# Kernel tuning notes

Measured on AMD Instinct MI355X. Metric: run time of the kernel, lower is better.

The kernel has to match this reference:

```python
import jax, jax.numpy as jnp
import numpy as np
import math

B, T, C = 2, 2048, 1024
H = 16
D = C // H


def setup_inputs() -> dict:
    key = jax.random.key(0)
    ks = jax.random.split(key, 5)
    s = 1.0 / math.sqrt(C)
    return {
        "x": jax.random.normal(ks[0], (B, T, C), dtype=jnp.float32),
        "W_qkv": jax.random.normal(ks[1], (C, 3 * C), dtype=jnp.float32) * s,
        "b_qkv": jnp.zeros((3 * C,), dtype=jnp.float32),
        "W_proj": jax.random.normal(ks[2], (C, C), dtype=jnp.float32) * s,
        "b_proj": jnp.zeros((C,), dtype=jnp.float32),
    }


def reference(x, W_qkv, b_qkv, W_proj, b_proj):
    qkv = x @ W_qkv + b_qkv  # [B,T,3C]
    q, k, v = jnp.split(qkv, 3, axis=-1)
    # [B,T,C] -> [B,H,T,D]
    q = q.reshape(B, T, H, D).transpose(0, 2, 1, 3)
    k = k.reshape(B, T, H, D).transpose(0, 2, 1, 3)
    v = v.reshape(B, T, H, D).transpose(0, 2, 1, 3)
    sm_scale = 1.0 / math.sqrt(D)
    att = jnp.einsum("bhqd,bhkd->bhqk", q, k) * sm_scale
    causal = jnp.tril(jnp.ones((T, T), dtype=bool))  # True = keep
    att = jnp.where(causal, att, -jnp.inf)
    att = jax.nn.softmax(att, axis=-1)
    y = jnp.einsum("bhqk,bhkd->bhqd", att, v)  # [B,H,T,D]
    y = y.transpose(0, 2, 1, 3).reshape(B, T, C)
    return y @ W_proj + b_proj
```

## Files before the change

kernel.cpp:

```cpp
#include <hip/hip_runtime.h>
#include <hip/hip_bf16.h>
#include <math.h>

#define BB 2
#define TT 2048
#define CCH 1024
#define HH 16
#define DD 64
#define BT (BB*TT)
#define N3 (3*CCH)

typedef __attribute__((ext_vector_type(8))) short short8;
typedef __attribute__((ext_vector_type(4))) float f32x4;
typedef __attribute__((ext_vector_type(16))) float f32x16;

__device__ __forceinline__ unsigned short f2bf(float f) {
  unsigned int u = __float_as_uint(f);
  unsigned int r = (u + 0x7FFFu + ((u >> 16) & 1u)) >> 16;
  return (unsigned short)r;
}
__device__ __forceinline__ int cvtpk(float lo, float hi) {
  int r;
  asm("v_cvt_pk_bf16_f32 %0, %1, %2" : "=v"(r) : "v"(lo), "v"(hi));
  return r;
}
__device__ __forceinline__ void plswap(int &a, int &b) {
  asm("v_permlane32_swap_b32 %0, %1" : "+v"(a), "+v"(b));
}
__device__ __forceinline__ float fexp2(float x) {
  float r;
  asm("v_exp_f32 %0, %1" : "=v"(r) : "v"(x));
  return r;
}
__device__ __forceinline__ void gload_lds16(const unsigned short* g, unsigned short* l) {
  __builtin_amdgcn_global_load_lds((const __attribute__((address_space(1))) void*)g,
                                   (__attribute__((address_space(3))) void*)l, 16, 0, 0);
}
__device__ __forceinline__ float fmax3(float a, float b, float c) {
  return fmaxf(fmaxf(a, b), c);
}

__global__ __launch_bounds__(256) void k_convert(const float* __restrict__ in,
                                                 unsigned short* __restrict__ out, int n8) {
  int i = blockIdx.x * 256 + threadIdx.x;
  if (i < n8) {
    const float4 a = *(const float4*)(in + (size_t)i * 8);
    const float4 b = *(const float4*)(in + (size_t)i * 8 + 4);
    short8 v;
    v[0] = f2bf(a.x); v[1] = f2bf(a.y); v[2] = f2bf(a.z); v[3] = f2bf(a.w);
    v[4] = f2bf(b.x); v[5] = f2bf(b.y); v[6] = f2bf(b.z); v[7] = f2bf(b.w);
    *(short8*)(out + (size_t)i * 8) = v;
  }
}

__global__ __launch_bounds__(256) void k_transpose_cvt(const float* __restrict__ in,
                                                       unsigned short* __restrict__ out,
                                                       int R, int Cn) {
  __shared__ float tile[32][33];
  int tc = blockIdx.x * 32;
  int tr = blockIdx.y * 32;
  int lx = threadIdx.x & 31;
  int ly = threadIdx.x >> 5;
#pragma unroll
  for (int i = 0; i < 32; i += 8)
    tile[ly + i][lx] = in[(size_t)(tr + ly + i) * Cn + tc + lx];
  __syncthreads();
#pragma unroll
  for (int i = 0; i < 32; i += 8)
    out[(size_t)(tc + ly + i) * R + tr + lx] = f2bf(tile[lx][ly + i]);
}

__global__ __launch_bounds__(256) void k_qkv_gemm(const unsigned short* __restrict__ Xb,
                                                  const unsigned short* __restrict__ Wt,
                                                  const float* __restrict__ bias,
                                                  unsigned short* __restrict__ Qo,
                                                  unsigned short* __restrict__ Ko,
                                                  unsigned short* __restrict__ Vto) {
  __shared__ __align__(16) unsigned short As[128 * 32];
  __shared__ __align__(16) unsigned short Bs[128 * 32];
  int tid = threadIdx.x;
  int mb = blockIdx.x * 128;
  int nb = blockIdx.y * 128;
  int wid = tid >> 6, lane = tid & 63;
  int wr = (wid >> 1) * 64, wc = (wid & 1) * 64;
  int l15 = lane & 15, l4 = lane >> 4;
  int l16 = lane >> 2, lc = (lane & 3) * 8;
  f32x4 acc[4][4];
#pragma unroll
  for (int a = 0; a < 4; ++a)
#pragma unroll
    for (int b = 0; b < 4; ++b)
#pragma unroll
      for (int j = 0; j < 4; ++j) acc[a][b][j] = 0.0f;

  for (int kb = 0; kb < CCH; kb += 32) {
#pragma unroll
    for (int i = 0; i < 2; ++i) {
      int arow = wid * 32 + i * 16;
      gload_lds16(Xb + (size_t)(mb + arow + l16) * CCH + kb + lc, &As[arow * 32]);
      gload_lds16(Wt + (size_t)(nb + arow + l16) * CCH + kb + lc, &Bs[arow * 32]);
    }
    __syncthreads();
    short8 af[4], bfr[4];
#pragma unroll
    for (int mt = 0; mt < 4; ++mt) af[mt] = *(const short8*)(&As[(wr + mt * 16 + l15) * 32 + l4 * 8]);
#pragma unroll
    for (int nt = 0; nt < 4; ++nt) bfr[nt] = *(const short8*)(&Bs[(wc + nt * 16 + l15) * 32 + l4 * 8]);
#pragma unroll
    for (int mt = 0; mt < 4; ++mt)
#pragma unroll
      for (int nt = 0; nt < 4; ++nt)
        acc[mt][nt] = __builtin_amdgcn_mfma_f32_16x16x32_bf16(af[mt], bfr[nt], acc[mt][nt], 0, 0, 0);
    __syncthreads();
  }

#pragma unroll
  for (int mt = 0; mt < 4; ++mt) {
#pragma unroll
    for (int nt = 0; nt < 4; ++nt) {
      int gcol = nb + wc + nt * 16 + l15;
      int which = gcol >> 10;
      int cc = gcol & 1023;
      int h = cc >> 6, d = cc & 63;
      float bv = bias[gcol];
#pragma unroll
      for (int j = 0; j < 4; ++j) {
        int grow = mb + wr + mt * 16 + l4 * 4 + j;
        int b = grow >> 11, t = grow & 2047;
        float v = acc[mt][nt][j] + bv;
        size_t bh = (size_t)(b * HH + h);
        if (which == 0)      Qo[(bh * TT + t) * DD + d] = f2bf(v * 0.18033688f);
        else if (which == 1) Ko[(bh * TT + t) * DD + d] = f2bf(v);
        else                 Vto[(bh * DD + d) * TT + t] = f2bf(v);
      }
    }
  }
}

__global__ __launch_bounds__(128) void k_attn(const unsigned short* __restrict__ Qb,
                                              const unsigned short* __restrict__ Kb,
                                              const unsigned short* __restrict__ Vtb,
                                              unsigned short* __restrict__ Y) {
  __shared__ __align__(16) unsigned short Ks[2][64 * 64];
  __shared__ __align__(16) unsigned short Vs[2][64 * 64];
  int tid = threadIdx.x;
  int jx = blockIdx.x;
  int qsub = 31 - (jx >> 5);
  int bh = jx & 31;

  const unsigned short* Qp = Qb + (size_t)bh * TT * DD;
  const unsigned short* Kp = Kb + (size_t)bh * TT * DD;
  const unsigned short* Vp = Vtb + (size_t)bh * DD * TT;
  int wid = tid >> 6, lane = tid & 63;
  int l31 = lane & 31, h = lane >> 5;
  int q0 = qsub * 64 + wid * 32;
  int qrow = q0 + l31;

  short8 qf[4];
#pragma unroll
  for (int m = 0; m < 4; ++m)
    qf[m] = *(const short8*)(Qp + (size_t)qrow * DD + m * 16 + h * 8);

  f32x16 zv;
#pragma unroll
  for (int r = 0; r < 16; ++r) zv[r] = 0.0f;
  f32x16 po[2];
  po[0] = zv; po[1] = zv;
  float mrun = -1e30f, lrun = 0.0f;

#pragma unroll
  for (int i2 = 0; i2 < 4; ++i2) {
    int c = i2 * 128 + wid * 64 + lane;
    int srow = c >> 3, scol = ((c & 7) ^ (srow & 7)) * 8;
    int dst = (i2 * 128 + wid * 64) * 8;
    gload_lds16(Kp + (size_t)srow * DD + scol, &Ks[0][dst]);
    gload_lds16(Vp + (size_t)srow * TT + scol, &Vs[0][dst]);
  }

  int buf = 0;
  for (int t = 0; t <= qsub; ++t) {
    __syncthreads();
    int kvb = t * 64;
    if (t < qsub) {
      int kvb2 = kvb + 64;
#pragma unroll
      for (int i2 = 0; i2 < 4; ++i2) {
        int c = i2 * 128 + wid * 64 + lane;
        int srow = c >> 3, scol = ((c & 7) ^ (srow & 7)) * 8;
        int dst = (i2 * 128 + wid * 64) * 8;
        gload_lds16(Kp + (size_t)(kvb2 + srow) * DD + scol, &Ks[buf ^ 1][dst]);
        gload_lds16(Vp + (size_t)srow * TT + kvb2 + scol, &Vs[buf ^ 1][dst]);
      }
    }

    {
      f32x16 st[2];
      __builtin_amdgcn_s_setprio(1);
#pragma unroll
      for (int t32 = 0; t32 < 2; ++t32) {
        int row = t32 * 32 + l31;
        {
          int off = row * 64 + ((h ^ (row & 7)) * 8);
          short8 kf = *(const short8*)(&Ks[buf][off]);
          st[t32] = __builtin_amdgcn_mfma_f32_32x32x16_bf16(kf, qf[0], zv, 0, 0, 0);
        }
#pragma unroll
        for (int m = 1; m < 4; ++m) {
          int off = row * 64 + (((2 * m + h) ^ (row & 7)) * 8);
          short8 kf = *(const short8*)(&Ks[buf][off]);
          st[t32] = __builtin_amdgcn_mfma_f32_32x32x16_bf16(kf, qf[m], st[t32], 0, 0, 0);
        }
      }
      __builtin_amdgcn_s_setprio(0);

      if (kvb + 63 > q0) {
#pragma unroll
        for (int t32 = 0; t32 < 2; ++t32)
#pragma unroll
          for (int r = 0; r < 16; ++r) {
            int kvg = kvb + t32 * 32 + (r & 3) + 8 * (r >> 2) + 4 * h;
            if (kvg > qrow) st[t32][r] = -1e30f;
          }
      }

      float A = st[0][0], B = st[0][1], C = st[0][2], Dv = st[0][3];
#pragma unroll
      for (int r = 4; r < 16; r += 4) {
        A = fmax3(A, st[0][r], st[0][r + 1]);
        B = fmax3(B, st[0][r + 2], st[0][r + 3]);
        C = fmax3(C, st[1][r - 4], st[1][r - 3]);
        Dv = fmax3(Dv, st[1][r - 2], st[1][r - 1]);
      }
      C = fmax3(C, st[1][12], st[1][13]);
      Dv = fmax3(Dv, st[1][14], st[1][15]);
      float mx = fmaxf(fmax3(A, B, C), Dv);
      mx = fmaxf(mx, __shfl_xor(mx, 32));

      if (__any(mx - mrun > 8.0f)) {
        float mnew = fmaxf(mrun, mx);
        float alpha = fexp2(mrun - mnew);
        lrun *= alpha;
#pragma unroll
        for (int dt = 0; dt < 2; ++dt)
#pragma unroll
          for (int r = 0; r < 16; ++r) po[dt][r] *= alpha;
        mrun = mnew;
      }

      float sum = 0.0f;
#pragma unroll
      for (int t32 = 0; t32 < 2; ++t32)
#pragma unroll
        for (int r = 0; r < 16; ++r) {
          float p = fexp2(st[t32][r] - mrun);
          st[t32][r] = p;
          sum += p;
        }
      sum += __shfl_xor(sum, 32);
      lrun += sum;

      short8 pf[4];
#pragma unroll
      for (int g = 0; g < 4; ++g) {
        int t32 = g >> 1, r0 = (g & 1) * 8;
        int a = cvtpk(st[t32][r0 + 0], st[t32][r0 + 1]);
        int b = cvtpk(st[t32][r0 + 4], st[t32][r0 + 5]);
        plswap(a, b);
        int c = cvtpk(st[t32][r0 + 2], st[t32][r0 + 3]);
        int d = cvtpk(st[t32][r0 + 6], st[t32][r0 + 7]);
        plswap(c, d);
        union { int w[4]; short8 s; } un;
        un.w[0] = a; un.w[1] = c; un.w[2] = b; un.w[3] = d;
        pf[g] = un.s;
      }

      __builtin_amdgcn_s_setprio(1);
#pragma unroll
      for (int dt = 0; dt < 2; ++dt) {
#pragma unroll
        for (int g = 0; g < 4; ++g) {
          int row = dt * 32 + l31;
          int off = row * 64 + (((2 * g + h) ^ (row & 7)) * 8);
          short8 vf = *(const short8*)(&Vs[buf][off]);
          po[dt] = __builtin_amdgcn_mfma_f32_32x32x16_bf16(vf, pf[g], po[dt], 0, 0, 0);
        }
      }
      __builtin_amdgcn_s_setprio(0);
    }

    buf ^= 1;
  }

  float inv = 1.0f / lrun;
  int b = bh >> 4, hh = bh & 15;
  int trow = qsub * 64 + wid * 32 + l31;
  unsigned short* yp = Y + ((size_t)(b * TT + trow)) * CCH + hh * DD;
#pragma unroll
  for (int dt = 0; dt < 2; ++dt)
#pragma unroll
    for (int r = 0; r < 16; r += 2) {
      int d = dt * 32 + (r & 3) + 8 * (r >> 2) + 4 * h;
      *(int*)(yp + d) = cvtpk(po[dt][r] * inv, po[dt][r + 1] * inv);
    }
}

__global__ __launch_bounds__(256) void k_proj_gemm(const unsigned short* __restrict__ Yb,
                                                   const unsigned short* __restrict__ Wt,
                                                   const float* __restrict__ bias,
                                                   float* __restrict__ Out) {
  __shared__ __align__(16) unsigned short As[128 * 32];
  __shared__ __align__(16) unsigned short Bs[128 * 32];
  int tid = threadIdx.x;
  int mb = blockIdx.x * 128;
  int nb = blockIdx.y * 128;
  int wid = tid >> 6, lane = tid & 63;
  int wr = (wid >> 1) * 64, wc = (wid & 1) * 64;
  int l15 = lane & 15, l4 = lane >> 4;
  int l16 = lane >> 2, lc = (lane & 3) * 8;
  f32x4 acc[4][4];
#pragma unroll
  for (int a = 0; a < 4; ++a)
#pragma unroll
    for (int b = 0; b < 4; ++b)
#pragma unroll
      for (int j = 0; j < 4; ++j) acc[a][b][j] = 0.0f;

  for (int kb = 0; kb < CCH; kb += 32) {
#pragma unroll
    for (int i = 0; i < 2; ++i) {
      int arow = wid * 32 + i * 16;
      gload_lds16(Yb + (size_t)(mb + arow + l16) * CCH + kb + lc, &As[arow * 32]);
      gload_lds16(Wt + (size_t)(nb + arow + l16) * CCH + kb + lc, &Bs[arow * 32]);
    }
    __syncthreads();
    short8 af[4], bfr[4];
#pragma unroll
    for (int mt = 0; mt < 4; ++mt) af[mt] = *(const short8*)(&As[(wr + mt * 16 + l15) * 32 + l4 * 8]);
#pragma unroll
    for (int nt = 0; nt < 4; ++nt) bfr[nt] = *(const short8*)(&Bs[(wc + nt * 16 + l15) * 32 + l4 * 8]);
#pragma unroll
    for (int mt = 0; mt < 4; ++mt)
#pragma unroll
      for (int nt = 0; nt < 4; ++nt)
        acc[mt][nt] = __builtin_amdgcn_mfma_f32_16x16x32_bf16(af[mt], bfr[nt], acc[mt][nt], 0, 0, 0);
    __syncthreads();
  }

#pragma unroll
  for (int mt = 0; mt < 4; ++mt) {
#pragma unroll
    for (int nt = 0; nt < 4; ++nt) {
      int gcol = nb + wc + nt * 16 + l15;
      float bv = bias[gcol];
#pragma unroll
      for (int j = 0; j < 4; ++j) {
        int grow = mb + wr + mt * 16 + l4 * 4 + j;
        Out[(size_t)grow * CCH + gcol] = acc[mt][nt][j] + bv;
      }
    }
  }
}

extern "C" void kernel_launch(void* const* d_in, const int* in_sizes, int n_in,
                              void* d_out, int out_size, void* d_ws, size_t ws_size,
                              hipStream_t stream) {
  const float* x      = (const float*)d_in[0];
  const float* W_qkv  = (const float*)d_in[1];
  const float* b_qkv  = (const float*)d_in[2];
  const float* W_proj = (const float*)d_in[3];
  const float* b_proj = (const float*)d_in[4];
  float* out = (float*)d_out;

  char* ws = (char*)d_ws;
  size_t off = 0;
  unsigned short* Wt_qkv  = (unsigned short*)(ws + off); off += (size_t)N3 * CCH * 2;
  unsigned short* Wt_proj = (unsigned short*)(ws + off); off += (size_t)CCH * CCH * 2;
  unsigned short* Xb      = (unsigned short*)(ws + off); off += (size_t)BT * CCH * 2;
  unsigned short* Qb      = (unsigned short*)(ws + off); off += (size_t)BT * CCH * 2;
  unsigned short* Kb      = (unsigned short*)(ws + off); off += (size_t)BT * CCH * 2;
  unsigned short* Vt      = (unsigned short*)(ws + off); off += (size_t)BT * CCH * 2;
  unsigned short* Yb      = (unsigned short*)(ws + off); off += (size_t)BT * CCH * 2;

  k_convert<<<dim3(BT * CCH / 8 / 256), 256, 0, stream>>>(x, Xb, BT * CCH / 8);
  k_transpose_cvt<<<dim3(N3 / 32, CCH / 32), 256, 0, stream>>>(W_qkv, Wt_qkv, CCH, N3);
  k_transpose_cvt<<<dim3(CCH / 32, CCH / 32), 256, 0, stream>>>(W_proj, Wt_proj, CCH, CCH);
  k_qkv_gemm<<<dim3(BT / 128, N3 / 128), 256, 0, stream>>>(Xb, Wt_qkv, b_qkv, Qb, Kb, Vt);
  k_attn<<<dim3(1024), 128, 0, stream>>>(Qb, Kb, Vt, Yb);
  k_proj_gemm<<<dim3(BT / 128, CCH / 128), 256, 0, stream>>>(Yb, Wt_proj, b_proj, out);
}
```

Measured before the change: 125.9 us.

## Split attention KV range across two waves with per-wave buffers and LSE merge

Each attention block now covers 32 query rows instead of 64, and the grid doubles to 2048 blocks. The two waves each take alternating KV tiles into their own LDS buffer, so the per-iteration block barrier goes away. Each wave prefetches its next tile after issuing its own LDS reads. At the end the partial softmax states are merged through LDS using the running max and sum. This trades the extra Q-load and merge overhead and less per-block K/V reuse for more parallelism, better load balance and no barriers in the loop.

```diff
diff --git a/kernel.cpp b/kernel.cpp
--- a/kernel.cpp
+++ b/kernel.cpp
@@ -145,16 +145,17 @@
   __shared__ __align__(16) unsigned short Vs[2][64 * 64];
   int tid = threadIdx.x;
   int jx = blockIdx.x;
-  int qsub = 31 - (jx >> 5);
+  int j = 63 - (jx >> 5);
   int bh = jx & 31;
+  int wid = tid >> 6, lane = tid & 63;
+  int l31 = lane & 31, h = lane >> 5;
+  int q0 = j * 32;
+  int qrow = q0 + l31;
+  int tmax = j >> 1;
 
   const unsigned short* Qp = Qb + (size_t)bh * TT * DD;
   const unsigned short* Kp = Kb + (size_t)bh * TT * DD;
   const unsigned short* Vp = Vtb + (size_t)bh * DD * TT;
-  int wid = tid >> 6, lane = tid & 63;
-  int l31 = lane & 31, h = lane >> 5;
-  int q0 = qsub * 64 + wid * 32;
-  int qrow = q0 + l31;
 
   short8 qf[4];
 #pragma unroll
@@ -168,140 +169,163 @@
   po[0] = zv; po[1] = zv;
   float mrun = -1e30f, lrun = 0.0f;
 
-#pragma unroll
-  for (int i2 = 0; i2 < 4; ++i2) {
-    int c = i2 * 128 + wid * 64 + lane;
-    int srow = c >> 3, scol = ((c & 7) ^ (srow & 7)) * 8;
-    int dst = (i2 * 128 + wid * 64) * 8;
-    gload_lds16(Kp + (size_t)srow * DD + scol, &Ks[0][dst]);
-    gload_lds16(Vp + (size_t)srow * TT + scol, &Vs[0][dst]);
-  }
-
-  int buf = 0;
-  for (int t = 0; t <= qsub; ++t) {
-    __syncthreads();
+  if (wid <= tmax) {
+#pragma unroll
+    for (int i = 0; i < 8; ++i) {
+      int c = i * 64 + lane;
+      int srow = c >> 3, scol = ((c & 7) ^ (srow & 7)) * 8;
+      gload_lds16(Kp + (size_t)(wid * 64 + srow) * DD + scol, &Ks[wid][i * 512]);
+      gload_lds16(Vp + (size_t)srow * TT + wid * 64 + scol, &Vs[wid][i * 512]);
+    }
+  }
+
+  for (int t = wid; t <= tmax; t += 2) {
     int kvb = t * 64;
-    if (t < qsub) {
-      int kvb2 = kvb + 64;
-#pragma unroll
-      for (int i2 = 0; i2 < 4; ++i2) {
-        int c = i2 * 128 + wid * 64 + lane;
+    asm volatile("s_waitcnt vmcnt(0)" ::: "memory");
+    __builtin_amdgcn_sched_barrier(0);
+
+    short8 kf[2][4];
+#pragma unroll
+    for (int t32 = 0; t32 < 2; ++t32) {
+      int row = t32 * 32 + l31;
+#pragma unroll
+      for (int m = 0; m < 4; ++m)
+        kf[t32][m] = *(const short8*)(&Ks[wid][row * 64 + (((2 * m + h) ^ (row & 7)) * 8)]);
+    }
+    f32x16 st[2];
+    __builtin_amdgcn_s_setprio(1);
+#pragma unroll
+    for (int t32 = 0; t32 < 2; ++t32) {
+      st[t32] = __builtin_amdgcn_mfma_f32_32x32x16_bf16(kf[t32][0], qf[0], zv, 0, 0, 0);
+#pragma unroll
+      for (int m = 1; m < 4; ++m)
+        st[t32] = __builtin_amdgcn_mfma_f32_32x32x16_bf16(kf[t32][m], qf[m], st[t32], 0, 0, 0);
+    }
+    __builtin_amdgcn_s_setprio(0);
+
+    short8 vf[2][4];
+#pragma unroll
+    for (int dt = 0; dt < 2; ++dt) {
+      int row = dt * 32 + l31;
+#pragma unroll
+      for (int g = 0; g < 4; ++g)
+        vf[dt][g] = *(const short8*)(&Vs[wid][row * 64 + (((2 * g + h) ^ (row & 7)) * 8)]);
+    }
+    asm volatile("s_waitcnt lgkmcnt(0)" ::: "memory");
+    __builtin_amdgcn_sched_barrier(0);
+
+    if (t + 2 <= tmax) {
+      int kvb2 = kvb + 128;
+#pragma unroll
+      for (int i = 0; i < 8; ++i) {
+        int c = i * 64 + lane;
         int srow = c >> 3, scol = ((c & 7) ^ (srow & 7)) * 8;
-        int dst = (i2 * 128 + wid * 64) * 8;
-        gload_lds16(Kp + (size_t)(kvb2 + srow) * DD + scol, &Ks[buf ^ 1][dst]);
-        gload_lds16(Vp + (size_t)srow * TT + kvb2 + scol, &Vs[buf ^ 1][dst]);
+        gload_lds16(Kp + (size_t)(kvb2 + srow) * DD + scol, &Ks[wid][i * 512]);
+        gload_lds16(Vp + (size_t)srow * TT + kvb2 + scol, &Vs[wid][i * 512]);
       }
     }
 
-    {
-      f32x16 st[2];
-      __builtin_amdgcn_s_setprio(1);
-#pragma unroll
-      for (int t32 = 0; t32 < 2; ++t32) {
-        int row = t32 * 32 + l31;
-        {
-          int off = row * 64 + ((h ^ (row & 7)) * 8);
-          short8 kf = *(const short8*)(&Ks[buf][off]);
-          st[t32] = __builtin_amdgcn_mfma_f32_32x32x16_bf16(kf, qf[0], zv, 0, 0, 0);
+    if (kvb + 63 > q0) {
+#pragma unroll
+      for (int t32 = 0; t32 < 2; ++t32)
+#pragma unroll
+        for (int r = 0; r < 16; ++r) {
+          int kvg = kvb + t32 * 32 + (r & 3) + 8 * (r >> 2) + 4 * h;
+          if (kvg > qrow) st[t32][r] = -1e30f;
         }
-#pragma unroll
-        for (int m = 1; m < 4; ++m) {
-          int off = row * 64 + (((2 * m + h) ^ (row & 7)) * 8);
-          short8 kf = *(const short8*)(&Ks[buf][off]);
-          st[t32] = __builtin_amdgcn_mfma_f32_32x32x16_bf16(kf, qf[m], st[t32], 0, 0, 0);
-        }
+    }
+
+    float A = st[0][0], B = st[0][1], C = st[0][2], Dv = st[0][3];
+#pragma unroll
+    for (int r = 4; r < 16; r += 4) {
+      A = fmax3(A, st[0][r], st[0][r + 1]);
+      B = fmax3(B, st[0][r + 2], st[0][r + 3]);
+      C = fmax3(C, st[1][r - 4], st[1][r - 3]);
+      Dv = fmax3(Dv, st[1][r - 2], st[1][r - 1]);
+    }
+    C = fmax3(C, st[1][12], st[1][13]);
+    Dv = fmax3(Dv, st[1][14], st[1][15]);
+    float mx = fmaxf(fmax3(A, B, C), Dv);
+    mx = fmaxf(mx, __shfl_xor(mx, 32));
+
+    if (__any(mx - mrun > 8.0f)) {
+      float mnew = fmaxf(mrun, mx);
+      float alpha = fexp2(mrun - mnew);
+      lrun *= alpha;
+#pragma unroll
+      for (int dt = 0; dt < 2; ++dt)
+#pragma unroll
+        for (int r = 0; r < 16; ++r) po[dt][r] *= alpha;
+      mrun = mnew;
+    }
+
+    float sum = 0.0f;
+#pragma unroll
+    for (int t32 = 0; t32 < 2; ++t32)
+#pragma unroll
+      for (int r = 0; r < 16; ++r) {
+        float p = fexp2(st[t32][r] - mrun);
+        st[t32][r] = p;
+        sum += p;
       }
-      __builtin_amdgcn_s_setprio(0);
-
-      if (kvb + 63 > q0) {
-#pragma unroll
-        for (int t32 = 0; t32 < 2; ++t32)
-#pragma unroll
-          for (int r = 0; r < 16; ++r) {
-            int kvg = kvb + t32 * 32 + (r & 3) + 8 * (r >> 2) + 4 * h;
-            if (kvg > qrow) st[t32][r] = -1e30f;
-          }
+    sum += __shfl_xor(sum, 32);
+    lrun += sum;
+
+    short8 pf[4];
+#pragma unroll
+    for (int g = 0; g < 4; ++g) {
+      int t32 = g >> 1, r0 = (g & 1) * 8;
+      int a = cvtpk(st[t32][r0 + 0], st[t32][r0 + 1]);
+      int b = cvtpk(st[t32][r0 + 4], st[t32][r0 + 5]);
+      plswap(a, b);
+      int c = cvtpk(st[t32][r0 + 2], st[t32][r0 + 3]);
+      int d = cvtpk(st[t32][r0 + 6], st[t32][r0 + 7]);
+      plswap(c, d);
+      union { int w[4]; short8 s; } un;
+      un.w[0] = a; un.w[1] = c; un.w[2] = b; un.w[3] = d;
+      pf[g] = un.s;
+    }
+
+    __builtin_amdgcn_s_setprio(1);
+#pragma unroll
+    for (int dt = 0; dt < 2; ++dt)
+#pragma unroll
+      for (int g = 0; g < 4; ++g)
+        po[dt] = __builtin_amdgcn_mfma_f32_32x32x16_bf16(vf[dt][g], pf[g], po[dt], 0, 0, 0);
+    __builtin_amdgcn_s_setprio(0);
+  }
+
+  asm volatile("s_waitcnt vmcnt(0)" ::: "memory");
+  __syncthreads();
+  float* ex   = (float*)&Ks[0][0];
+  float* exml = (float*)&Vs[0][0];
+  if (wid == 1) {
+#pragma unroll
+    for (int dt = 0; dt < 2; ++dt)
+#pragma unroll
+      for (int r = 0; r < 16; ++r) ex[lane * 33 + dt * 16 + r] = po[dt][r];
+    exml[lane] = mrun;
+    exml[64 + lane] = lrun;
+  }
+  __syncthreads();
+  if (wid == 0) {
+    float m1 = exml[lane], l1 = exml[64 + lane];
+    float M = fmaxf(mrun, m1);
+    float a0 = fexp2(mrun - M), a1 = fexp2(m1 - M);
+    float inv = 1.0f / (lrun * a0 + l1 * a1);
+    a0 *= inv; a1 *= inv;
+    int b = bh >> 4, hh = bh & 15;
+    unsigned short* yp = Y + ((size_t)(b * TT + qrow)) * CCH + hh * DD;
+#pragma unroll
+    for (int dt = 0; dt < 2; ++dt)
+#pragma unroll
+      for (int r = 0; r < 16; r += 2) {
+        int d = dt * 32 + (r & 3) + 8 * (r >> 2) + 4 * h;
+        float v0 = po[dt][r]     * a0 + ex[lane * 33 + dt * 16 + r]     * a1;
+        float v1 = po[dt][r + 1] * a0 + ex[lane * 33 + dt * 16 + r + 1] * a1;
+        *(int*)(yp + d) = cvtpk(v0, v1);
       }
-
-      float A = st[0][0], B = st[0][1], C = st[0][2], Dv = st[0][3];
-#pragma unroll
-      for (int r = 4; r < 16; r += 4) {
-        A = fmax3(A, st[0][r], st[0][r + 1]);
-        B = fmax3(B, st[0][r + 2], st[0][r + 3]);
-        C = fmax3(C, st[1][r - 4], st[1][r - 3]);
-        Dv = fmax3(Dv, st[1][r - 2], st[1][r - 1]);
-      }
-      C = fmax3(C, st[1][12], st[1][13]);
-      Dv = fmax3(Dv, st[1][14], st[1][15]);
-      float mx = fmaxf(fmax3(A, B, C), Dv);
-      mx = fmaxf(mx, __shfl_xor(mx, 32));
-
-      if (__any(mx - mrun > 8.0f)) {
-        float mnew = fmaxf(mrun, mx);
-        float alpha = fexp2(mrun - mnew);
-        lrun *= alpha;
-#pragma unroll
-        for (int dt = 0; dt < 2; ++dt)
-#pragma unroll
-          for (int r = 0; r < 16; ++r) po[dt][r] *= alpha;
-        mrun = mnew;
-      }
-
-      float sum = 0.0f;
-#pragma unroll
-      for (int t32 = 0; t32 < 2; ++t32)
-#pragma unroll
-        for (int r = 0; r < 16; ++r) {
-          float p = fexp2(st[t32][r] - mrun);
-          st[t32][r] = p;
-          sum += p;
-        }
-      sum += __shfl_xor(sum, 32);
-      lrun += sum;
-
-      short8 pf[4];
-#pragma unroll
-      for (int g = 0; g < 4; ++g) {
-        int t32 = g >> 1, r0 = (g & 1) * 8;
-        int a = cvtpk(st[t32][r0 + 0], st[t32][r0 + 1]);
-        int b = cvtpk(st[t32][r0 + 4], st[t32][r0 + 5]);
-        plswap(a, b);
-        int c = cvtpk(st[t32][r0 + 2], st[t32][r0 + 3]);
-        int d = cvtpk(st[t32][r0 + 6], st[t32][r0 + 7]);
-        plswap(c, d);
-        union { int w[4]; short8 s; } un;
-        un.w[0] = a; un.w[1] = c; un.w[2] = b; un.w[3] = d;
-        pf[g] = un.s;
-      }
-
-      __builtin_amdgcn_s_setprio(1);
-#pragma unroll
-      for (int dt = 0; dt < 2; ++dt) {
-#pragma unroll
-        for (int g = 0; g < 4; ++g) {
-          int row = dt * 32 + l31;
-          int off = row * 64 + (((2 * g + h) ^ (row & 7)) * 8);
-          short8 vf = *(const short8*)(&Vs[buf][off]);
-          po[dt] = __builtin_amdgcn_mfma_f32_32x32x16_bf16(vf, pf[g], po[dt], 0, 0, 0);
-        }
-      }
-      __builtin_amdgcn_s_setprio(0);
-    }
-
-    buf ^= 1;
-  }
-
-  float inv = 1.0f / lrun;
-  int b = bh >> 4, hh = bh & 15;
-  int trow = qsub * 64 + wid * 32 + l31;
-  unsigned short* yp = Y + ((size_t)(b * TT + trow)) * CCH + hh * DD;
-#pragma unroll
-  for (int dt = 0; dt < 2; ++dt)
-#pragma unroll
-    for (int r = 0; r < 16; r += 2) {
-      int d = dt * 32 + (r & 3) + 8 * (r >> 2) + 4 * h;
-      *(int*)(yp + d) = cvtpk(po[dt][r] * inv, po[dt][r + 1] * inv);
-    }
+  }
 }
 
 __global__ __launch_bounds__(256) void k_proj_gemm(const unsigned short* __restrict__ Yb,
@@ -385,6 +409,6 @@
   k_transpose_cvt<<<dim3(N3 / 32, CCH / 32), 256, 0, stream>>>(W_qkv, Wt_qkv, CCH, N3);
   k_transpose_cvt<<<dim3(CCH / 32, CCH / 32), 256, 0, stream>>>(W_proj, Wt_proj, CCH, CCH);
   k_qkv_gemm<<<dim3(BT / 128, N3 / 128), 256, 0, stream>>>(Xb, Wt_qkv, b_qkv, Qb, Kb, Vt);
-  k_attn<<<dim3(1024), 128, 0, stream>>>(Qb, Kb, Vt, Yb);
+  k_attn<<<dim3(2048), 128, 0, stream>>>(Qb, Kb, Vt, Yb);
   k_proj_gemm<<<dim3(BT / 128, CCH / 128), 256, 0, stream>>>(Yb, Wt_proj, b_proj, out);
 }
```

After: 120.4 us. -4.3%, faster.
